# Kernel optimization log

Hardware: AMD Instinct MI355X
Metric: run time of the kernel (lower is better)

## Reference

```python
import jax, jax.numpy as jnp
import numpy as np
from jax import lax

B, C, H, W_DIM, K = 8, 256, 128, 128, 64


def setup_inputs() -> dict:
    key = jax.random.key(0)
    k1, k2, k3, k4 = jax.random.split(key, 4)
    x = jax.random.normal(k1, (B, C, H, W_DIM), dtype=jnp.float32)
    index = jax.random.randint(k2, (B, H, W_DIM), 0, K)
    stdv = 1.0 / np.sqrt(C)
    W = jax.random.uniform(k3, (C, C), minval=-stdv, maxval=stdv, dtype=jnp.float32)
    conv_w = jax.random.normal(k4, (C, C, 1, 1), dtype=jnp.float32) * stdv
    return {"x": x, "index": index, "W": W, "conv_w": conv_w}


def reference(x, index, W, conv_w):
    # one-hot segment membership (B,H,W,K) -- replaces scatter_ + broadcast in torch
    onehot = jax.nn.one_hot(index, K, dtype=x.dtype)
    counts = jnp.sum(onehot, axis=(1, 2))                       # (B,K)
    sums = jnp.einsum('bhwk,bchw->bkc', onehot, x)              # segment sums
    denom = counts + (counts == 0).astype(x.dtype)              # avoid div by 0
    means = sums / denom[..., None]                             # (B,K,C)

    # Mahalanobis-style pairwise adjacency: adj[b,i,j] = exp(-d^T (W W^T) d)
    M = W @ W.T                                                 # (C,C)
    diff = means[:, None, :, :] - means[:, :, None, :]          # (B,K,K,C): means[b,j]-means[b,i]
    quad = jnp.einsum('bijc,cd,bijd->bij', diff, M, diff)
    adj = jnp.exp(-quad)
    adj = adj * (1.0 - jnp.eye(K, dtype=x.dtype))               # zero diagonal

    # adjacency-weighted message aggregation over segments
    agg = jnp.einsum('bij,bjc->bic', adj, means)                # (B,K,C)

    # scatter messages back to pixels by segment id (each pixel belongs to 1 segment)
    gathered = agg[jnp.arange(B)[:, None, None], index]         # (B,H,W,C)
    features = x + jnp.transpose(gathered, (0, 3, 1, 2))        # (B,C,H,W)

    # 1x1 conv, no bias
    out = lax.conv_general_dilated(features, conv_w, window_strides=(1, 1),
                                   padding='VALID',
                                   dimension_numbers=('NCHW', 'OIHW', 'NCHW'))
    return out
```

## Files before the change

kernel.cpp:

```cpp
#include <hip/hip_runtime.h>
#include <cstdint>
#include <cstddef>

#define B_  8
#define C_  256
#define HW_ 16384
#define K_  64

__global__ __launch_bounds__(256) void k_zero(float* __restrict__ p, int n) {
    int i = blockIdx.x * 256 + threadIdx.x;
    if (i < n) p[i] = 0.f;
}

__global__ __launch_bounds__(256) void k_scatter(const float* __restrict__ x,
                                                 const int* __restrict__ idx,
                                                 float* __restrict__ sums,
                                                 float* __restrict__ counts) {
    __shared__ float lsum[K_ * C_];
    __shared__ int   sidx[256];
    __shared__ float lcnt[K_];
    const int tid = threadIdx.x;
    const int b = blockIdx.y;
    const int p0 = blockIdx.x * 256;

    float4 z4 = make_float4(0.f, 0.f, 0.f, 0.f);
    for (int i = tid; i < K_ * C_ / 4; i += 256) ((float4*)lsum)[i] = z4;
    if (tid < K_) lcnt[tid] = 0.f;
    sidx[tid] = idx[b * HW_ + p0 + tid];
    __syncthreads();

    atomicAdd(&lcnt[sidx[tid]], 1.f);

    const int c = tid;
    const float4* xr = (const float4*)(x + ((size_t)b * C_ + c) * HW_ + p0);
    #pragma unroll 4
    for (int p4 = 0; p4 < 64; ++p4) {
        float4 v = xr[p4];
        int k0 = sidx[p4 * 4 + 0];
        int k1 = sidx[p4 * 4 + 1];
        int k2 = sidx[p4 * 4 + 2];
        int k3 = sidx[p4 * 4 + 3];
        atomicAdd(&lsum[k0 * C_ + c], v.x);
        atomicAdd(&lsum[k1 * C_ + c], v.y);
        atomicAdd(&lsum[k2 * C_ + c], v.z);
        atomicAdd(&lsum[k3 * C_ + c], v.w);
    }
    __syncthreads();

    for (int k = 0; k < K_; ++k)
        atomicAdd(&sums[((size_t)b * K_ + k) * C_ + c], lsum[k * C_ + c]);
    if (tid < K_) atomicAdd(&counts[b * K_ + tid], lcnt[tid]);
}

__global__ __launch_bounds__(256) void k_prep(const float* __restrict__ sums,
                                              const float* __restrict__ counts,
                                              const float* __restrict__ Wm,
                                              const float* __restrict__ convw,
                                              float* __restrict__ means,
                                              float* __restrict__ Mm,
                                              float* __restrict__ cwT) {
    const int bx = blockIdx.x, t = threadIdx.x;
    __shared__ float wl[C_];
    if (bx < B_ * K_) {
        float cnt = counts[bx];
        float denom = cnt + (cnt == 0.f ? 1.f : 0.f);
        means[(size_t)bx * C_ + t] = sums[(size_t)bx * C_ + t] / denom;
    } else if (bx < B_ * K_ + C_) {
        int cr = bx - B_ * K_;
        wl[t] = Wm[cr * C_ + t];
        __syncthreads();
        float acc = 0.f;
        for (int e = 0; e < C_; ++e) acc += wl[e] * Wm[t * C_ + e];
        Mm[cr * C_ + t] = acc;
    } else {
        int cr = bx - (B_ * K_ + C_);
        cwT[cr * C_ + t] = convw[t * C_ + cr];
    }
}

__global__ __launch_bounds__(256) void k_P(const float* __restrict__ means,
                                           const float* __restrict__ Mm,
                                           float* __restrict__ P) {
    const int bi = blockIdx.x;
    const int d = threadIdx.x;
    __shared__ float ml[C_];
    ml[d] = means[(size_t)bi * C_ + d];
    __syncthreads();
    float acc = 0.f;
    for (int cc = 0; cc < C_; ++cc) acc += ml[cc] * Mm[cc * C_ + d];
    P[(size_t)bi * C_ + d] = acc;
}

__global__ __launch_bounds__(256) void k_G(const float* __restrict__ P,
                                           const float* __restrict__ means,
                                           float* __restrict__ G) {
    const int bi = blockIdx.x;
    const int b = bi >> 6;
    const int t = threadIdx.x;
    __shared__ float pl[C_];
    pl[t] = P[(size_t)bi * C_ + t];
    __syncthreads();
    const int j = t >> 2, q = t & 3;
    const float* mj = means + ((size_t)b * K_ + j) * C_ + q * 64;
    const float* pq = pl + q * 64;
    float acc = 0.f;
    for (int d = 0; d < 64; ++d) acc += pq[d] * mj[d];
    acc += __shfl_xor(acc, 1);
    acc += __shfl_xor(acc, 2);
    if (q == 0) G[(size_t)bi * K_ + j] = acc;
}

__global__ __launch_bounds__(256) void k_agg(const float* __restrict__ G,
                                             const float* __restrict__ means,
                                             float* __restrict__ agg) {
    const int bi = blockIdx.x;
    const int b = bi >> 6, i = bi & 63;
    const int t = threadIdx.x;
    __shared__ float adjl[K_];
    if (t < K_) {
        int j = t;
        float Gii = G[(size_t)bi * K_ + i];
        float Gjj = G[((size_t)b * K_ + j) * K_ + j];
        float Gij = G[(size_t)bi * K_ + j];
        float quad = Gii + Gjj - 2.f * Gij;
        adjl[j] = (j == i) ? 0.f : expf(-quad);
    }
    __syncthreads();
    float acc = 0.f;
    for (int j = 0; j < K_; ++j)
        acc += adjl[j] * means[((size_t)b * K_ + j) * C_ + t];
    agg[(size_t)bi * C_ + t] = acc;
}

__global__ __launch_bounds__(256) void k_proj(const float* __restrict__ agg,
                                              const float* __restrict__ cwT,
                                              float* __restrict__ proj) {
    const int bk = blockIdx.x;
    const int o = threadIdx.x;
    __shared__ float al[C_];
    al[o] = agg[(size_t)bk * C_ + o];
    __syncthreads();
    float acc = 0.f;
    for (int cc = 0; cc < C_; ++cc) acc += al[cc] * cwT[cc * C_ + o];
    proj[(size_t)bk * C_ + o] = acc;
}

#define BM 128
#define BN 128
#define BKK 32
__global__ __launch_bounds__(256) void k_gemm(const float* __restrict__ x,
                                              const int* __restrict__ idx,
                                              const float* __restrict__ cwT,
                                              const float* __restrict__ proj,
                                              float* __restrict__ out) {
    __shared__ float As[BKK][BM];
    __shared__ float Bs[BKK][BN];
    const int tid = threadIdx.x;
    const int o0 = blockIdx.x * BM;
    const int p0 = blockIdx.y * BN;
    const int b = blockIdx.z;

    float acc[8][8];
    #pragma unroll
    for (int i = 0; i < 8; ++i)
        #pragma unroll
        for (int j = 0; j < 8; ++j) acc[i][j] = 0.f;

    const float4* cwT4 = (const float4*)cwT;
    const float4* x4 = (const float4*)(x + (size_t)b * C_ * HW_);

    const int tm4 = (tid & 15) * 4;
    const int tn4 = (tid >> 4) * 4;

    for (int kt = 0; kt < C_; kt += BKK) {
        #pragma unroll
        for (int it = 0; it < 4; ++it) {
            int li = tid + it * 256;
            int row = li >> 5, col4 = li & 31;
            ((float4*)As)[li] = cwT4[(size_t)(kt + row) * (C_ / 4) + o0 / 4 + col4];
            ((float4*)Bs)[li] = x4[(size_t)(kt + row) * (HW_ / 4) + p0 / 4 + col4];
        }
        __syncthreads();
        #pragma unroll
        for (int kk = 0; kk < BKK; ++kk) {
            float4 a0 = *(const float4*)&As[kk][tm4];
            float4 a1 = *(const float4*)&As[kk][tm4 + 64];
            float4 b0 = *(const float4*)&Bs[kk][tn4];
            float4 b1 = *(const float4*)&Bs[kk][tn4 + 64];
            float av[8] = {a0.x, a0.y, a0.z, a0.w, a1.x, a1.y, a1.z, a1.w};
            float bv[8] = {b0.x, b0.y, b0.z, b0.w, b1.x, b1.y, b1.z, b1.w};
            #pragma unroll
            for (int i = 0; i < 8; ++i)
                #pragma unroll
                for (int j = 0; j < 8; ++j)
                    acc[i][j] += av[i] * bv[j];
        }
        __syncthreads();
    }

    int kp[8];
    #pragma unroll
    for (int j = 0; j < 8; ++j) {
        int col = (j < 4) ? (tn4 + j) : (64 + tn4 + j - 4);
        kp[j] = idx[b * HW_ + p0 + col];
    }
    #pragma unroll
    for (int i = 0; i < 8; ++i) {
        const int o = o0 + ((i < 4) ? (tm4 + i) : (64 + tm4 + i - 4));
        float r[8];
        #pragma unroll
        for (int j = 0; j < 8; ++j)
            r[j] = acc[i][j] + proj[((size_t)b * K_ + kp[j]) * C_ + o];
        float* orow = out + ((size_t)b * C_ + o) * HW_ + p0;
        *(float4*)(orow + tn4)      = make_float4(r[0], r[1], r[2], r[3]);
        *(float4*)(orow + 64 + tn4) = make_float4(r[4], r[5], r[6], r[7]);
    }
}

extern "C" void kernel_launch(void* const* d_in, const int* in_sizes, int n_in,
                              void* d_out, int out_size, void* d_ws, size_t ws_size,
                              hipStream_t stream) {
    const float* x     = (const float*)d_in[0];
    const int*   idx   = (const int*)d_in[1];
    const float* Wm    = (const float*)d_in[2];
    const float* convw = (const float*)d_in[3];
    float* out = (float*)d_out;
    float* wsf = (float*)d_ws;

    const size_t N_SUMS = (size_t)B_ * K_ * C_;
    const size_t N_CNT  = (size_t)B_ * K_;
    const size_t N_M    = (size_t)C_ * C_;
    const size_t N_G    = (size_t)B_ * K_ * K_;

    float* proj = wsf;
    float* cwT  = wsf + N_SUMS;

    const size_t earlyN = N_SUMS + N_CNT + N_SUMS + N_M + N_SUMS + N_G + N_SUMS;
    const size_t needAll = (N_SUMS + N_M + earlyN) * sizeof(float);
    float* early = (ws_size >= needAll) ? (wsf + N_SUMS + N_M)
                                        : (out + (size_t)16 * 1024 * 1024);

    float* sums   = early;
    float* counts = sums + N_SUMS;
    float* means  = counts + N_CNT;
    float* Mm     = means + N_SUMS;
    float* P      = Mm + N_M;
    float* G      = P + N_SUMS;
    float* agg    = G + N_G;

    k_zero<<<dim3(514), dim3(256), 0, stream>>>(sums, (int)(N_SUMS + N_CNT));
    k_scatter<<<dim3(64, 8), dim3(256), 0, stream>>>(x, idx, sums, counts);
    k_prep<<<dim3(512 + 256 + 256), dim3(256), 0, stream>>>(sums, counts, Wm, convw,
                                                            means, Mm, cwT);
    k_P<<<dim3(512), dim3(256), 0, stream>>>(means, Mm, P);
    k_G<<<dim3(512), dim3(256), 0, stream>>>(P, means, G);
    k_agg<<<dim3(512), dim3(256), 0, stream>>>(G, means, agg);
    k_proj<<<dim3(512), dim3(256), 0, stream>>>(agg, cwT, proj);
    k_gemm<<<dim3(2, HW_ / BN, B_), dim3(256), 0, stream>>>(x, idx, cwT, proj, out);
}
```

Measured before the change: 576.2 us.

## Use split-bf16 MFMA for 1x1 conv GEMM and deterministic partial-sum reduction

The main GEMM moves from scalar FP32 FMAs to bf16 MFMA instructions. Each operand is split into a high and a low bf16 part, and three MFMAs per tile approximate FP32 accuracy. The segment scatter now writes per-block partials that a new reduce kernel sums, replacing global atomics and the zero-fill kernel. The pairwise quadratic form is computed directly from differences to avoid cancellation. The GEMM adds conversion work inside the loop and stores outputs with poorly coalesced scalar writes, and the 3-term bf16 split slightly reduces precision.

```diff
diff --git a/kernel.cpp b/kernel.cpp
--- a/kernel.cpp
+++ b/kernel.cpp
@@ -7,21 +7,29 @@
 #define HW_ 16384
 #define K_  64
 
-__global__ __launch_bounds__(256) void k_zero(float* __restrict__ p, int n) {
-    int i = blockIdx.x * 256 + threadIdx.x;
-    if (i < n) p[i] = 0.f;
+typedef __attribute__((ext_vector_type(8))) short bf16x8;
+typedef __attribute__((ext_vector_type(4))) float f32x4;
+
+__device__ __forceinline__ unsigned f2bf(float f) {
+    unsigned u = __builtin_bit_cast(unsigned, f);
+    return (u + 0x7FFFu + ((u >> 16) & 1u)) >> 16;
+}
+__device__ __forceinline__ float bf2f(unsigned h) {
+    unsigned u = h << 16;
+    return __builtin_bit_cast(float, u);
 }
 
 __global__ __launch_bounds__(256) void k_scatter(const float* __restrict__ x,
                                                  const int* __restrict__ idx,
-                                                 float* __restrict__ sums,
-                                                 float* __restrict__ counts) {
+                                                 float* __restrict__ part,
+                                                 float* __restrict__ pcnt) {
     __shared__ float lsum[K_ * C_];
     __shared__ int   sidx[256];
     __shared__ float lcnt[K_];
     const int tid = threadIdx.x;
     const int b = blockIdx.y;
-    const int p0 = blockIdx.x * 256;
+    const int pb = blockIdx.x;
+    const int p0 = pb * 256;
 
     float4 z4 = make_float4(0.f, 0.f, 0.f, 0.f);
     for (int i = tid; i < K_ * C_ / 4; i += 256) ((float4*)lsum)[i] = z4;
@@ -47,33 +55,53 @@
     }
     __syncthreads();
 
+    const size_t pbg = (size_t)b * 64 + pb;
+    float* dst = part + (pbg * K_) * C_;
     for (int k = 0; k < K_; ++k)
-        atomicAdd(&sums[((size_t)b * K_ + k) * C_ + c], lsum[k * C_ + c]);
-    if (tid < K_) atomicAdd(&counts[b * K_ + tid], lcnt[tid]);
-}
-
-__global__ __launch_bounds__(256) void k_prep(const float* __restrict__ sums,
-                                              const float* __restrict__ counts,
-                                              const float* __restrict__ Wm,
+        dst[k * C_ + c] = lsum[k * C_ + c];
+    if (tid < K_) pcnt[pbg * K_ + tid] = lcnt[tid];
+}
+
+__global__ __launch_bounds__(256) void k_reduce(const float* __restrict__ part,
+                                                const float* __restrict__ pcnt,
+                                                float* __restrict__ means) {
+    const int bk = blockIdx.x;
+    const int b = bk >> 6, k = bk & 63;
+    const int c = threadIdx.x;
+    __shared__ float cnt_s;
+
+    if (c < 64) {
+        float cl = pcnt[((size_t)b * 64 + c) * K_ + k];
+        #pragma unroll
+        for (int off = 32; off; off >>= 1) cl += __shfl_down(cl, off);
+        if (c == 0) cnt_s = cl;
+    }
+    __syncthreads();
+    const float cnt = cnt_s;
+    const float denom = cnt + (cnt == 0.f ? 1.f : 0.f);
+
+    float acc = 0.f;
+    #pragma unroll 4
+    for (int pb = 0; pb < 64; ++pb)
+        acc += part[(((size_t)b * 64 + pb) * K_ + k) * C_ + c];
+    means[(size_t)bk * C_ + c] = acc / denom;
+}
+
+__global__ __launch_bounds__(256) void k_prep(const float* __restrict__ Wm,
                                               const float* __restrict__ convw,
-                                              float* __restrict__ means,
                                               float* __restrict__ Mm,
                                               float* __restrict__ cwT) {
     const int bx = blockIdx.x, t = threadIdx.x;
     __shared__ float wl[C_];
-    if (bx < B_ * K_) {
-        float cnt = counts[bx];
-        float denom = cnt + (cnt == 0.f ? 1.f : 0.f);
-        means[(size_t)bx * C_ + t] = sums[(size_t)bx * C_ + t] / denom;
-    } else if (bx < B_ * K_ + C_) {
-        int cr = bx - B_ * K_;
+    if (bx < C_) {
+        int cr = bx;
         wl[t] = Wm[cr * C_ + t];
         __syncthreads();
         float acc = 0.f;
         for (int e = 0; e < C_; ++e) acc += wl[e] * Wm[t * C_ + e];
         Mm[cr * C_ + t] = acc;
     } else {
-        int cr = bx - (B_ * K_ + C_);
+        int cr = bx - C_;
         cwT[cr * C_ + t] = convw[t * C_ + cr];
     }
 }
@@ -97,14 +125,20 @@
     const int bi = blockIdx.x;
     const int b = bi >> 6;
     const int t = threadIdx.x;
-    __shared__ float pl[C_];
+    __shared__ float pl[C_], ml[C_];
     pl[t] = P[(size_t)bi * C_ + t];
+    ml[t] = means[(size_t)bi * C_ + t];
     __syncthreads();
     const int j = t >> 2, q = t & 3;
+    const float* Pj = P + ((size_t)b * K_ + j) * C_ + q * 64;
     const float* mj = means + ((size_t)b * K_ + j) * C_ + q * 64;
     const float* pq = pl + q * 64;
-    float acc = 0.f;
-    for (int d = 0; d < 64; ++d) acc += pq[d] * mj[d];
+    const float* mq = ml + q * 64;
+    float acc = 0.f;
+    for (int d0 = 0; d0 < 64; ++d0) {
+        int d = (d0 + q * 16) & 63;
+        acc += (pq[d] - Pj[d]) * (mq[d] - mj[d]);
+    }
     acc += __shfl_xor(acc, 1);
     acc += __shfl_xor(acc, 2);
     if (q == 0) G[(size_t)bi * K_ + j] = acc;
@@ -119,10 +153,7 @@
     __shared__ float adjl[K_];
     if (t < K_) {
         int j = t;
-        float Gii = G[(size_t)bi * K_ + i];
-        float Gjj = G[((size_t)b * K_ + j) * K_ + j];
-        float Gij = G[(size_t)bi * K_ + j];
-        float quad = Gii + Gjj - 2.f * Gij;
+        float quad = G[(size_t)bi * K_ + j];
         adjl[j] = (j == i) ? 0.f : expf(-quad);
     }
     __syncthreads();
@@ -148,72 +179,118 @@
 #define BM 128
 #define BN 128
 #define BKK 32
+#define STRD 80
+
 __global__ __launch_bounds__(256) void k_gemm(const float* __restrict__ x,
                                               const int* __restrict__ idx,
-                                              const float* __restrict__ cwT,
+                                              const float* __restrict__ convw,
                                               const float* __restrict__ proj,
                                               float* __restrict__ out) {
-    __shared__ float As[BKK][BM];
-    __shared__ float Bs[BKK][BN];
+    __shared__ float Xf[BKK][BN];
+    __shared__ __align__(16) unsigned char AsH[BM * STRD];
+    __shared__ __align__(16) unsigned char AsL[BM * STRD];
+    __shared__ __align__(16) unsigned char BsH[BN * STRD];
+    __shared__ __align__(16) unsigned char BsL[BN * STRD];
+
     const int tid = threadIdx.x;
     const int o0 = blockIdx.x * BM;
     const int p0 = blockIdx.y * BN;
-    const int b = blockIdx.z;
-
-    float acc[8][8];
+    const int b  = blockIdx.z;
+
+    const int lane = tid & 63;
+    const int wv = tid >> 6;
+    const int wo = (wv >> 1) * 64, wp = (wv & 1) * 64;
+    const int lr = lane & 15, lg = lane >> 4;
+
+    f32x4 acc[4][4];
     #pragma unroll
-    for (int i = 0; i < 8; ++i)
-        #pragma unroll
-        for (int j = 0; j < 8; ++j) acc[i][j] = 0.f;
-
-    const float4* cwT4 = (const float4*)cwT;
+    for (int i = 0; i < 4; ++i)
+        #pragma unroll
+        for (int j = 0; j < 4; ++j) acc[i][j] = (f32x4){0.f, 0.f, 0.f, 0.f};
+
+    const float4* w4 = (const float4*)convw;
     const float4* x4 = (const float4*)(x + (size_t)b * C_ * HW_);
-
-    const int tm4 = (tid & 15) * 4;
-    const int tn4 = (tid >> 4) * 4;
 
     for (int kt = 0; kt < C_; kt += BKK) {
         #pragma unroll
         for (int it = 0; it < 4; ++it) {
             int li = tid + it * 256;
-            int row = li >> 5, col4 = li & 31;
-            ((float4*)As)[li] = cwT4[(size_t)(kt + row) * (C_ / 4) + o0 / 4 + col4];
-            ((float4*)Bs)[li] = x4[(size_t)(kt + row) * (HW_ / 4) + p0 / 4 + col4];
+            {
+                int row = li >> 3, c4 = li & 7;
+                float4 v = w4[(size_t)(o0 + row) * (C_ / 4) + (kt >> 2) + c4];
+                unsigned h0 = f2bf(v.x), h1 = f2bf(v.y), h2 = f2bf(v.z), h3 = f2bf(v.w);
+                unsigned l0 = f2bf(v.x - bf2f(h0)), l1 = f2bf(v.y - bf2f(h1));
+                unsigned l2 = f2bf(v.z - bf2f(h2)), l3 = f2bf(v.w - bf2f(h3));
+                uint2 hv, lv;
+                hv.x = h0 | (h1 << 16); hv.y = h2 | (h3 << 16);
+                lv.x = l0 | (l1 << 16); lv.y = l2 | (l3 << 16);
+                *(uint2*)&AsH[row * STRD + c4 * 8] = hv;
+                *(uint2*)&AsL[row * STRD + c4 * 8] = lv;
+            }
+            {
+                int row = li >> 5, c4 = li & 31;
+                *(float4*)&Xf[row][c4 * 4] =
+                    x4[(size_t)(kt + row) * (HW_ / 4) + (p0 >> 2) + c4];
+            }
         }
         __syncthreads();
         #pragma unroll
-        for (int kk = 0; kk < BKK; ++kk) {
-            float4 a0 = *(const float4*)&As[kk][tm4];
-            float4 a1 = *(const float4*)&As[kk][tm4 + 64];
-            float4 b0 = *(const float4*)&Bs[kk][tn4];
-            float4 b1 = *(const float4*)&Bs[kk][tn4 + 64];
-            float av[8] = {a0.x, a0.y, a0.z, a0.w, a1.x, a1.y, a1.z, a1.w};
-            float bv[8] = {b0.x, b0.y, b0.z, b0.w, b1.x, b1.y, b1.z, b1.w};
+        for (int it = 0; it < 2; ++it) {
+            int id = tid + it * 256;
+            int p = id & 127, cg = id >> 7;
+            unsigned hh[8], ll[8];
             #pragma unroll
-            for (int i = 0; i < 8; ++i)
-                #pragma unroll
-                for (int j = 0; j < 8; ++j)
-                    acc[i][j] += av[i] * bv[j];
+            for (int j = 0; j < 8; ++j) {
+                float v = Xf[cg * 8 + j][p];
+                unsigned h = f2bf(v);
+                hh[j] = h;
+                ll[j] = f2bf(v - bf2f(h));
+            }
+            uint4 hv, lv;
+            hv.x = hh[0] | (hh[1] << 16); hv.y = hh[2] | (hh[3] << 16);
+            hv.z = hh[4] | (hh[5] << 16); hv.w = hh[6] | (hh[7] << 16);
+            lv.x = ll[0] | (ll[1] << 16); lv.y = ll[2] | (ll[3] << 16);
+            lv.z = ll[4] | (ll[5] << 16); lv.w = ll[6] | (ll[7] << 16);
+            *(uint4*)&BsH[p * STRD + cg * 16] = hv;
+            *(uint4*)&BsL[p * STRD + cg * 16] = lv;
         }
         __syncthreads();
-    }
-
-    int kp[8];
+        bf16x8 ah[4], al[4];
+        #pragma unroll
+        for (int mt = 0; mt < 4; ++mt) {
+            int off = (wo + mt * 16 + lr) * STRD + lg * 16;
+            ah[mt] = *(const bf16x8*)&AsH[off];
+            al[mt] = *(const bf16x8*)&AsL[off];
+        }
+        #pragma unroll
+        for (int nt = 0; nt < 4; ++nt) {
+            int off = (wp + nt * 16 + lr) * STRD + lg * 16;
+            bf16x8 bh = *(const bf16x8*)&BsH[off];
+            bf16x8 bl = *(const bf16x8*)&BsL[off];
+            #pragma unroll
+            for (int mt = 0; mt < 4; ++mt) {
+                acc[mt][nt] = __builtin_amdgcn_mfma_f32_16x16x32_bf16(ah[mt], bh, acc[mt][nt], 0, 0, 0);
+                acc[mt][nt] = __builtin_amdgcn_mfma_f32_16x16x32_bf16(ah[mt], bl, acc[mt][nt], 0, 0, 0);
+                acc[mt][nt] = __builtin_amdgcn_mfma_f32_16x16x32_bf16(al[mt], bh, acc[mt][nt], 0, 0, 0);
+            }
+        }
+        __syncthreads();
+    }
+
     #pragma unroll
-    for (int j = 0; j < 8; ++j) {
-        int col = (j < 4) ? (tn4 + j) : (64 + tn4 + j - 4);
-        kp[j] = idx[b * HW_ + p0 + col];
-    }
-    #pragma unroll
-    for (int i = 0; i < 8; ++i) {
-        const int o = o0 + ((i < 4) ? (tm4 + i) : (64 + tm4 + i - 4));
-        float r[8];
-        #pragma unroll
-        for (int j = 0; j < 8; ++j)
-            r[j] = acc[i][j] + proj[((size_t)b * K_ + kp[j]) * C_ + o];
-        float* orow = out + ((size_t)b * C_ + o) * HW_ + p0;
-        *(float4*)(orow + tn4)      = make_float4(r[0], r[1], r[2], r[3]);
-        *(float4*)(orow + 64 + tn4) = make_float4(r[4], r[5], r[6], r[7]);
+    for (int nt = 0; nt < 4; ++nt) {
+        const int p = p0 + wp + nt * 16 + lr;
+        const int kp = idx[b * HW_ + p];
+        const float* pr = proj + ((size_t)b * K_ + kp) * C_;
+        #pragma unroll
+        for (int mt = 0; mt < 4; ++mt) {
+            const int ob = o0 + wo + mt * 16 + lg * 4;
+            #pragma unroll
+            for (int r = 0; r < 4; ++r) {
+                const int o = ob + r;
+                out[((size_t)b * C_ + o) * HW_ + p] = acc[mt][nt][r] + pr[o];
+            }
+        }
     }
 }
 
@@ -227,34 +304,35 @@
     float* out = (float*)d_out;
     float* wsf = (float*)d_ws;
 
-    const size_t N_SUMS = (size_t)B_ * K_ * C_;
-    const size_t N_CNT  = (size_t)B_ * K_;
+    const size_t N_PART = (size_t)B_ * 64 * K_ * C_;
+    const size_t N_PCNT = (size_t)B_ * 64 * K_;
+    const size_t N_MEAN = (size_t)B_ * K_ * C_;
     const size_t N_M    = (size_t)C_ * C_;
     const size_t N_G    = (size_t)B_ * K_ * K_;
+    const size_t outN   = (size_t)B_ * C_ * HW_;
 
     float* proj = wsf;
-    float* cwT  = wsf + N_SUMS;
-
-    const size_t earlyN = N_SUMS + N_CNT + N_SUMS + N_M + N_SUMS + N_G + N_SUMS;
-    const size_t needAll = (N_SUMS + N_M + earlyN) * sizeof(float);
-    float* early = (ws_size >= needAll) ? (wsf + N_SUMS + N_M)
-                                        : (out + (size_t)16 * 1024 * 1024);
-
-    float* sums   = early;
-    float* counts = sums + N_SUMS;
-    float* means  = counts + N_CNT;
-    float* Mm     = means + N_SUMS;
-    float* P      = Mm + N_M;
-    float* G      = P + N_SUMS;
-    float* agg    = G + N_G;
-
-    k_zero<<<dim3(514), dim3(256), 0, stream>>>(sums, (int)(N_SUMS + N_CNT));
-    k_scatter<<<dim3(64, 8), dim3(256), 0, stream>>>(x, idx, sums, counts);
-    k_prep<<<dim3(512 + 256 + 256), dim3(256), 0, stream>>>(sums, counts, Wm, convw,
-                                                            means, Mm, cwT);
+    float* cwT  = wsf + N_MEAN;
+
+    const size_t earlyN = N_PART + N_PCNT + N_MEAN + N_M + N_MEAN + N_G + N_MEAN;
+    const size_t needAll = (N_MEAN + N_M + earlyN) * sizeof(float);
+    float* early = (ws_size >= needAll) ? (wsf + N_MEAN + N_M)
+                                        : (out + (outN - earlyN));
+
+    float* part  = early;
+    float* pcnt  = part + N_PART;
+    float* means = pcnt + N_PCNT;
+    float* Mm    = means + N_MEAN;
+    float* P     = Mm + N_M;
+    float* G     = P + N_MEAN;
+    float* agg   = G + N_G;
+
+    k_scatter<<<dim3(64, 8), dim3(256), 0, stream>>>(x, idx, part, pcnt);
+    k_reduce<<<dim3(512), dim3(256), 0, stream>>>(part, pcnt, means);
+    k_prep<<<dim3(512), dim3(256), 0, stream>>>(Wm, convw, Mm, cwT);
     k_P<<<dim3(512), dim3(256), 0, stream>>>(means, Mm, P);
     k_G<<<dim3(512), dim3(256), 0, stream>>>(P, means, G);
     k_agg<<<dim3(512), dim3(256), 0, stream>>>(G, means, agg);
     k_proj<<<dim3(512), dim3(256), 0, stream>>>(agg, cwT, proj);
-    k_gemm<<<dim3(2, HW_ / BN, B_), dim3(256), 0, stream>>>(x, idx, cwT, proj, out);
-}
+    k_gemm<<<dim3(2, HW_ / BN, B_), dim3(256), 0, stream>>>(x, idx, convw, proj, out);
+}
```

New measurement: 522.7 us. 9.3% less time.
